# Kernel optimization log

Hardware: AMD Instinct MI355X
Metric: run time of the kernel (lower is better)

## Reference

```python
import jax, jax.numpy as jnp
import numpy as np

N, CIN, COUT, H, W, K = 2, 64, 64, 256, 512, 3


def _gen_sphere_position(height, width, Kh, Kw):
    # Faithful numpy port of SphereConv.gen_sphere_position (ERP type).
    delta_lat = np.pi / height
    delta_lon = 2 * np.pi / width
    range_x = np.arange(-(Kw // 2), Kw // 2 + 1)
    if not Kw % 2:
        range_x = np.delete(range_x, Kw // 2)
    range_y = np.arange(-(Kh // 2), Kh // 2 + 1)
    if not Kh % 2:
        range_y = np.delete(range_y, Kh // 2)
    kerX = np.tan(range_x * delta_lon)
    kerY = np.tan(range_y * delta_lat) / np.cos(range_y * delta_lon)
    kerX, kerY = np.meshgrid(kerX, kerY)
    rho = np.sqrt(kerX ** 2 + kerY ** 2)
    if Kh % 2 and Kw % 2:
        rho[Kh // 2][Kw // 2] = 1e-08
    nu = np.arctan(rho)
    cos_nu, sin_nu = np.cos(nu), np.sin(nu)
    lat_range = (np.arange(height) / height - 0.5) * np.pi
    lon_range = (np.arange(width) / width - 0.5) * (2 * np.pi)
    lat = np.array([np.arcsin(cos_nu * np.sin(l) + kerY * sin_nu * np.cos(l) / rho) for l in lat_range])  # (H,Kh,Kw)
    lat = np.array([lat for _ in lon_range]).transpose((1, 0, 2, 3))  # (H,W,Kh,Kw)
    lon = np.array([np.arctan2(kerX * sin_nu, rho * np.cos(l) * cos_nu - kerY * np.sin(l) * sin_nu) for l in lat_range])  # (H,Kh,Kw)
    lon = np.array([lon + _lon for _lon in lon_range]).transpose((1, 0, 2, 3))  # (H,W,Kh,Kw)
    lat = (lat / np.pi + 0.5) * height
    lon = (lon / (2 * np.pi) + 0.5) * width % width
    LatLon = np.stack((lat, lon)).astype(np.float32)  # (2,H,W,Kh,Kw)
    LatLon = LatLon.transpose((3, 4, 0, 1, 2)).reshape(Kh * Kw * 2, height, width)  # channel = (i*Kw+j)*2 + {0:lat,1:lon}
    return LatLon


def setup_inputs() -> dict:
    key = jax.random.key(0)
    kx, kw = jax.random.split(key)
    x = jax.random.normal(kx, (N, CIN, H, W), dtype=jnp.float32)
    n = CIN * K * K
    stdv = 1.0 / np.sqrt(n)
    weight = jax.random.uniform(kw, (COUT, CIN, K, K), dtype=jnp.float32, minval=-stdv, maxval=stdv)
    position = jnp.asarray(_gen_sphere_position(H, W, K, K))  # (2*K*K, H, W)
    return {"x": x, "weight": weight, "position": position}


def _sphere_conv(x, weight, position):
    # x: [N,C,H,W]; position: [2*K2,Hout,Wout] absolute (lat=y, lon=x) sample coords per kernel tap.
    Cout, Cin, Kh, Kw = weight.shape
    K2 = Kh * Kw
    Hi, Wi = x.shape[2], x.shape[3]
    pos = position.reshape(K2, 2, position.shape[-2], position.shape[-1])
    py, px = pos[:, 0], pos[:, 1]  # [K2,Hout,Wout]
    y0 = jnp.floor(py)
    x0 = jnp.floor(px)
    dy = py - y0
    dx = px - x0

    def corner(yi, xi, wgt):
        valid = (yi >= 0) & (yi <= Hi - 1) & (xi >= 0) & (xi <= Wi - 1)
        yc = jnp.clip(yi, 0, Hi - 1).astype(jnp.int32)
        xc = jnp.clip(xi, 0, Wi - 1).astype(jnp.int32)
        v = x[:, :, yc, xc]  # gather -> [N,C,K2,Hout,Wout]
        return v * (wgt * valid)[None, None]

    sampled = (corner(y0, x0, (1 - dy) * (1 - dx))
               + corner(y0, x0 + 1, (1 - dy) * dx)
               + corner(y0 + 1, x0, dy * (1 - dx))
               + corner(y0 + 1, x0 + 1, dy * dx))  # [N,C,K2,Hout,Wout]
    w = weight.reshape(Cout, Cin, K2)
    return jnp.einsum('ock,nckhw->nohw', w, sampled)


def reference(x, weight, position):
    return _sphere_conv(x, weight, position)
```

## Files before the change

### kernel.cpp

```cpp
#include <hip/hip_runtime.h>
#include <hip/hip_bf16.h>


constexpr int N_ = 2;
constexpr int CIN = 64;
constexpr int COUT = 64;
constexpr int H_ = 256;
constexpr int W_ = 512;
constexpr int K2 = 9;
constexpr int HW = H_ * W_;
constexpr int NSTEP = (CIN * K2) / 32;
constexpr int PTILE = 128;
constexpr int SROW = 40;

typedef __attribute__((ext_vector_type(8))) short short8;
typedef __attribute__((ext_vector_type(4))) float floatx4;

__device__ __forceinline__ float bf2f(ushort u) {
  return __uint_as_float(((unsigned)u) << 16);
}

__global__ void prep_w(const float* __restrict__ w, ushort* __restrict__ wTr) {
  int i = blockIdx.x * blockDim.x + threadIdx.x;
  if (i >= 4 * NSTEP * 64 * 8) return;
  int j = i & 7;
  int lane = (i >> 3) & 63;
  int s = (i >> 9) % NSTEP;
  int wv = i / (512 * NSTEP);
  int o = wv * 16 + (lane & 15);
  int kk = s * 32 + (lane >> 4) * 8 + j;
  int tap = kk >> 6, c = kk & 63;
  __hip_bfloat16 b = __float2bfloat16(w[(o * CIN + c) * K2 + tap]);
  wTr[i] = *(ushort*)&b;
}

__global__ __launch_bounds__(256) void transpose_x(
    const float* __restrict__ x, ushort* __restrict__ xt) {
  __shared__ ushort tile[64 * 72];
  int b = blockIdx.x;
  int n = b >> 11;
  int hw0 = (b & 2047) * 64;
  int tid = threadIdx.x;
  int px = tid & 63, c4 = tid >> 6;
  const float* xn = x + (size_t)n * CIN * HW;
#pragma unroll
  for (int it = 0; it < 16; ++it) {
    int c = it * 4 + c4;
    float v = xn[(size_t)c * HW + hw0 + px];
    __hip_bfloat16 hb = __float2bfloat16(v);
    tile[px * 72 + c] = *(ushort*)&hb;
  }
  __syncthreads();
  ushort* xtn = xt + (size_t)n * HW * CIN;
#pragma unroll
  for (int it = 0; it < 2; ++it) {
    int task = it * 256 + tid;
    int px2 = task >> 3, chunk = task & 7;
    uint4 v = *(uint4*)&tile[px2 * 72 + chunk * 8];
    *(uint4*)&xtn[(size_t)(hw0 + px2) * 64 + chunk * 8] = v;
  }
}

__global__ __launch_bounds__(256, 4) void sphere_conv_mfma(
    const ushort* __restrict__ xt, const ushort* __restrict__ wTr,
    const float* __restrict__ pos, float* __restrict__ out) {
  __shared__ int off_lds[K2 * PTILE];
  __shared__ float4 wgt_lds[K2 * PTILE];
  __shared__ ushort sbuf[PTILE * SROW];

  int tid = threadIdx.x;
  int blk = blockIdx.x;
  int n = blk >> 10;
  int ptile = (blk & 1023) * PTILE;

  for (int i = tid; i < K2 * PTILE; i += 256) {
    int t = i / PTILE, p = i - t * PTILE;
    int hw = ptile + p;
    float py = pos[(2 * t + 0) * HW + hw];
    float px = pos[(2 * t + 1) * HW + hw];
    float y0f = floorf(py), x0f = floorf(px);
    float dy = py - y0f, dx = px - x0f;
    float y1f = y0f + 1.f, x1f = x0f + 1.f;
    float vy0 = (y0f >= 0.f && y0f <= (float)(H_ - 1)) ? 1.f : 0.f;
    float vy1 = (y1f >= 0.f && y1f <= (float)(H_ - 1)) ? 1.f : 0.f;
    float vx0 = (x0f >= 0.f && x0f <= (float)(W_ - 1)) ? 1.f : 0.f;
    float vx1 = (x1f >= 0.f && x1f <= (float)(W_ - 1)) ? 1.f : 0.f;
    float w00 = (1.f - dy) * (1.f - dx) * vy0 * vx0;
    float w01 = (1.f - dy) * dx * vy0 * vx1;
    float w10 = dy * (1.f - dx) * vy1 * vx0;
    float w11 = dy * dx * vy1 * vx1;
    int y0c = (int)fminf(fmaxf(y0f, 0.f), (float)(H_ - 1));
    int y1c = (int)fminf(fmaxf(y1f, 0.f), (float)(H_ - 1));
    int x0c = (int)fminf(fmaxf(x0f, 0.f), (float)(W_ - 1));
    int x1c = (int)fminf(fmaxf(x1f, 0.f), (float)(W_ - 1));
    int o00 = y0c * W_ + x0c;
    int dx1 = x1c - x0c;
    int dy1 = y1c - y0c;
    off_lds[i] = o00 | (dx1 << 20) | (dy1 << 21);
    wgt_lds[i] = make_float4(w00, w01, w10, w11);
  }

  int lane = tid & 63, wv = tid >> 6;
  int col = lane & 15, quad = lane >> 4;
  int px_s = tid >> 1, hf = tid & 1;

  floatx4 acc[8];
#pragma unroll
  for (int nt = 0; nt < 8; ++nt) acc[nt] = (floatx4)0.f;

  const ushort* xtn = xt + (size_t)n * HW * CIN;

  __syncthreads();

  for (int s = 0; s < NSTEP; ++s) {
    short8 afrag = *(const short8*)(wTr + ((wv * NSTEP + s) * 64 + lane) * 8);

    int t = s >> 1;
    int c0 = (s & 1) * 32 + hf * 16;
    int pk = off_lds[t * PTILE + px_s];
    float4 wgt = wgt_lds[t * PTILE + px_s];
    int o00 = pk & 0x1FFFF;
    int dx1 = (pk >> 20) & 1;
    int dyW = ((pk >> 21) & 1) * W_;
    const ushort* base = xtn + c0;
    const ushort* p00 = base + (size_t)o00 * 64;
    const ushort* p01 = base + (size_t)(o00 + dx1) * 64;
    const ushort* p10 = base + (size_t)(o00 + dyW) * 64;
    const ushort* p11 = base + (size_t)(o00 + dyW + dx1) * 64;
    short8 v0a = *(const short8*)p00, v0b = *(const short8*)(p00 + 8);
    short8 v1a = *(const short8*)p01, v1b = *(const short8*)(p01 + 8);
    short8 v2a = *(const short8*)p10, v2b = *(const short8*)(p10 + 8);
    short8 v3a = *(const short8*)p11, v3b = *(const short8*)(p11 + 8);

    float sv[16];
#pragma unroll
    for (int j = 0; j < 8; ++j) {
      sv[j]     = wgt.x * bf2f((ushort)v0a[j]);
      sv[8 + j] = wgt.x * bf2f((ushort)v0b[j]);
      sv[j]     = fmaf(wgt.y, bf2f((ushort)v1a[j]), sv[j]);
      sv[8 + j] = fmaf(wgt.y, bf2f((ushort)v1b[j]), sv[8 + j]);
      sv[j]     = fmaf(wgt.z, bf2f((ushort)v2a[j]), sv[j]);
      sv[8 + j] = fmaf(wgt.z, bf2f((ushort)v2b[j]), sv[8 + j]);
      sv[j]     = fmaf(wgt.w, bf2f((ushort)v3a[j]), sv[j]);
      sv[8 + j] = fmaf(wgt.w, bf2f((ushort)v3b[j]), sv[8 + j]);
    }
    __align__(16) ushort tmp[16];
#pragma unroll
    for (int j = 0; j < 16; ++j) {
      __hip_bfloat16 hb = __float2bfloat16(sv[j]);
      tmp[j] = *(ushort*)&hb;
    }
    uint4* dst = (uint4*)&sbuf[px_s * SROW + hf * 16];
    dst[0] = ((const uint4*)tmp)[0];
    dst[1] = ((const uint4*)tmp)[1];
    __syncthreads();

#pragma unroll
    for (int nt = 0; nt < 8; ++nt) {
      short8 bfrag = *(const short8*)&sbuf[(nt * 16 + col) * SROW + quad * 8];
      acc[nt] = __builtin_amdgcn_mfma_f32_16x16x32_bf16(afrag, bfrag, acc[nt], 0, 0, 0);
    }
    __syncthreads();
  }

#pragma unroll
  for (int nt = 0; nt < 8; ++nt) {
#pragma unroll
    for (int r = 0; r < 4; ++r) {
      int o = wv * 16 + quad * 4 + r;
      out[(size_t)(n * COUT + o) * HW + ptile + nt * 16 + col] = acc[nt][r];
    }
  }
}

extern "C" void kernel_launch(void* const* d_in, const int* in_sizes, int n_in,
                              void* d_out, int out_size, void* d_ws, size_t ws_size,
                              hipStream_t stream) {
  const float* x   = (const float*)d_in[0];
  const float* w   = (const float*)d_in[1];
  const float* pos = (const float*)d_in[2];
  float* out = (float*)d_out;

  ushort* wTr = (ushort*)d_ws;
  ushort* xt = (ushort*)((char*)d_ws + (128 << 10));

  prep_w<<<(4 * NSTEP * 64 * 8 + 255) / 256, 256, 0, stream>>>(w, wTr);
  transpose_x<<<N_ * (HW / 64), 256, 0, stream>>>(x, xt);

  int nblk = N_ * (HW / PTILE);
  sphere_conv_mfma<<<nblk, 256, 0, stream>>>(xt, wTr, pos, out);
}
```

Measured before the change: 210.8 us.

## Software-pipeline bilinear gathers with double-buffered LDS and packed bf16 math

Prefetches the next step's four-corner gathers into registers while the current step blends and runs the MFMAs. The LDS staging buffer is double-buffered so one barrier per step replaces two. Bilinear weights are stored as packed bf16 and blended with two-wide float FMAs, and the loop is fully unrolled. The extra registers for the prefetch are why the occupancy hint drops from 4 to 3 blocks, and bf16 weights lose some precision.

```diff
diff --git a/kernel.cpp b/kernel.cpp
--- a/kernel.cpp
+++ b/kernel.cpp
@@ -15,9 +15,10 @@
 
 typedef __attribute__((ext_vector_type(8))) short short8;
 typedef __attribute__((ext_vector_type(4))) float floatx4;
-
-__device__ __forceinline__ float bf2f(ushort u) {
-  return __uint_as_float(((unsigned)u) << 16);
+typedef __attribute__((ext_vector_type(2))) float floatx2;
+
+__device__ __forceinline__ float bfhi2f(unsigned u) {
+  return __uint_as_float(u);
 }
 
 __global__ void prep_w(const float* __restrict__ w, ushort* __restrict__ wTr) {
@@ -61,12 +62,12 @@
   }
 }
 
-__global__ __launch_bounds__(256, 4) void sphere_conv_mfma(
+__global__ __launch_bounds__(256, 3) void sphere_conv_mfma(
     const ushort* __restrict__ xt, const ushort* __restrict__ wTr,
     const float* __restrict__ pos, float* __restrict__ out) {
   __shared__ int off_lds[K2 * PTILE];
-  __shared__ float4 wgt_lds[K2 * PTILE];
-  __shared__ ushort sbuf[PTILE * SROW];
+  __shared__ uint2 wgt_lds[K2 * PTILE];
+  __shared__ ushort sbuf[2][PTILE * SROW];
 
   int tid = threadIdx.x;
   int blk = blockIdx.x;
@@ -94,10 +95,12 @@
     int x0c = (int)fminf(fmaxf(x0f, 0.f), (float)(W_ - 1));
     int x1c = (int)fminf(fmaxf(x1f, 0.f), (float)(W_ - 1));
     int o00 = y0c * W_ + x0c;
-    int dx1 = x1c - x0c;
-    int dy1 = y1c - y0c;
-    off_lds[i] = o00 | (dx1 << 20) | (dy1 << 21);
-    wgt_lds[i] = make_float4(w00, w01, w10, w11);
+    off_lds[i] = o00 | ((x1c - x0c) << 20) | ((y1c - y0c) << 21);
+    __hip_bfloat16 b00 = __float2bfloat16(w00), b01 = __float2bfloat16(w01);
+    __hip_bfloat16 b10 = __float2bfloat16(w10), b11 = __float2bfloat16(w11);
+    unsigned lo = ((unsigned)*(ushort*)&b01 << 16) | *(ushort*)&b00;
+    unsigned hi = ((unsigned)*(ushort*)&b11 << 16) | *(ushort*)&b10;
+    wgt_lds[i] = make_uint2(lo, hi);
   }
 
   int lane = tid & 63, wv = tid >> 6;
@@ -112,55 +115,81 @@
 
   __syncthreads();
 
-  for (int s = 0; s < NSTEP; ++s) {
-    short8 afrag = *(const short8*)(wTr + ((wv * NSTEP + s) * 64 + lane) * 8);
-
+  auto gather = [&](int s, short8 g[8], float w4[4]) {
     int t = s >> 1;
-    int c0 = (s & 1) * 32 + hf * 16;
+    int c0 = ((s & 1) << 5) + (hf << 4);
     int pk = off_lds[t * PTILE + px_s];
-    float4 wgt = wgt_lds[t * PTILE + px_s];
+    uint2 wr = wgt_lds[t * PTILE + px_s];
+    w4[0] = bfhi2f(wr.x << 16);
+    w4[1] = bfhi2f(wr.x & 0xFFFF0000u);
+    w4[2] = bfhi2f(wr.y << 16);
+    w4[3] = bfhi2f(wr.y & 0xFFFF0000u);
     int o00 = pk & 0x1FFFF;
     int dx1 = (pk >> 20) & 1;
     int dyW = ((pk >> 21) & 1) * W_;
     const ushort* base = xtn + c0;
     const ushort* p00 = base + (size_t)o00 * 64;
-    const ushort* p01 = base + (size_t)(o00 + dx1) * 64;
-    const ushort* p10 = base + (size_t)(o00 + dyW) * 64;
-    const ushort* p11 = base + (size_t)(o00 + dyW + dx1) * 64;
-    short8 v0a = *(const short8*)p00, v0b = *(const short8*)(p00 + 8);
-    short8 v1a = *(const short8*)p01, v1b = *(const short8*)(p01 + 8);
-    short8 v2a = *(const short8*)p10, v2b = *(const short8*)(p10 + 8);
-    short8 v3a = *(const short8*)p11, v3b = *(const short8*)(p11 + 8);
-
-    float sv[16];
-#pragma unroll
-    for (int j = 0; j < 8; ++j) {
-      sv[j]     = wgt.x * bf2f((ushort)v0a[j]);
-      sv[8 + j] = wgt.x * bf2f((ushort)v0b[j]);
-      sv[j]     = fmaf(wgt.y, bf2f((ushort)v1a[j]), sv[j]);
-      sv[8 + j] = fmaf(wgt.y, bf2f((ushort)v1b[j]), sv[8 + j]);
-      sv[j]     = fmaf(wgt.z, bf2f((ushort)v2a[j]), sv[j]);
-      sv[8 + j] = fmaf(wgt.z, bf2f((ushort)v2b[j]), sv[8 + j]);
-      sv[j]     = fmaf(wgt.w, bf2f((ushort)v3a[j]), sv[j]);
-      sv[8 + j] = fmaf(wgt.w, bf2f((ushort)v3b[j]), sv[8 + j]);
-    }
-    __align__(16) ushort tmp[16];
-#pragma unroll
-    for (int j = 0; j < 16; ++j) {
-      __hip_bfloat16 hb = __float2bfloat16(sv[j]);
-      tmp[j] = *(ushort*)&hb;
-    }
-    uint4* dst = (uint4*)&sbuf[px_s * SROW + hf * 16];
+    const ushort* p01 = p00 + dx1 * 64;
+    const ushort* p10 = p00 + dyW * 64;
+    const ushort* p11 = p10 + dx1 * 64;
+    g[0] = *(const short8*)p00; g[1] = *(const short8*)(p00 + 8);
+    g[2] = *(const short8*)p01; g[3] = *(const short8*)(p01 + 8);
+    g[4] = *(const short8*)p10; g[5] = *(const short8*)(p10 + 8);
+    g[6] = *(const short8*)p11; g[7] = *(const short8*)(p11 + 8);
+  };
+
+  short8 gA[8];
+  float wA[4];
+  gather(0, gA, wA);
+
+#pragma unroll
+  for (int s = 0; s < NSTEP; ++s) {
+    short8 gB[8];
+    float wB[4];
+    if (s + 1 < NSTEP) gather(s + 1, gB, wB);
+
+    const unsigned* u = (const unsigned*)gA;
+    floatx2 a2[8];
+#pragma unroll
+    for (int d = 0; d < 8; ++d) {
+      floatx2 f = {bfhi2f(u[d] << 16), bfhi2f(u[d] & 0xFFFF0000u)};
+      a2[d] = floatx2{wA[0], wA[0]} * f;
+    }
+#pragma unroll
+    for (int c = 1; c < 4; ++c) {
+#pragma unroll
+      for (int d = 0; d < 8; ++d) {
+        unsigned v = u[c * 8 + d];
+        floatx2 f = {bfhi2f(v << 16), bfhi2f(v & 0xFFFF0000u)};
+        a2[d] = __builtin_elementwise_fma(floatx2{wA[c], wA[c]}, f, a2[d]);
+      }
+    }
+    __align__(16) unsigned tmp[8];
+#pragma unroll
+    for (int d = 0; d < 8; ++d) {
+      __hip_bfloat16 lo = __float2bfloat16(a2[d].x);
+      __hip_bfloat16 hi = __float2bfloat16(a2[d].y);
+      tmp[d] = ((unsigned)*(ushort*)&hi << 16) | *(ushort*)&lo;
+    }
+    uint4* dst = (uint4*)&sbuf[s & 1][px_s * SROW + hf * 16];
     dst[0] = ((const uint4*)tmp)[0];
     dst[1] = ((const uint4*)tmp)[1];
+
     __syncthreads();
 
+    short8 afrag = *(const short8*)(wTr + ((wv * NSTEP + s) * 64 + lane) * 8);
 #pragma unroll
     for (int nt = 0; nt < 8; ++nt) {
-      short8 bfrag = *(const short8*)&sbuf[(nt * 16 + col) * SROW + quad * 8];
+      short8 bfrag = *(const short8*)&sbuf[s & 1][(nt * 16 + col) * SROW + quad * 8];
       acc[nt] = __builtin_amdgcn_mfma_f32_16x16x32_bf16(afrag, bfrag, acc[nt], 0, 0, 0);
     }
-    __syncthreads();
+
+    if (s + 1 < NSTEP) {
+#pragma unroll
+      for (int q = 0; q < 8; ++q) gA[q] = gB[q];
+#pragma unroll
+      for (int q = 0; q < 4; ++q) wA[q] = wB[q];
+    }
   }
 
 #pragma unroll
```

Result: no change. 210.5 us (-0.2%).
